# Optimization experiments

Measured on AMD Instinct MI355X. Metric: run time of the kernel, lower is better.

## Reference

```python
import jax, jax.numpy as jnp
import numpy as np

S, B, D, H = 512, 2048, 64, 128  # seqLength, batchSize, inputDim, hiddenDim


def setup_inputs() -> dict:
    key = jax.random.key(0)
    ks = jax.random.split(key, 6)
    return {
        "x": jax.random.normal(ks[0], (S, B, D), dtype=jnp.float32),
        "h0": jax.random.normal(ks[1], (B, H), dtype=jnp.float32) * 0.1,
        # nn.Linear(64,128) params
        "W_ih": jax.random.normal(ks[2], (H, D), dtype=jnp.float32) / np.sqrt(D).astype(np.float32),
        "b_ih": jax.random.normal(ks[3], (H,), dtype=jnp.float32) * 0.01,
        # nn.Linear(128,128) params
        "W_hh": jax.random.normal(ks[4], (H, H), dtype=jnp.float32) / np.sqrt(H).astype(np.float32),
        "b_hh": jax.random.normal(ks[5], (H,), dtype=jnp.float32) * 0.01,
    }


def reference(x, h0, W_ih, b_ih, W_hh, b_hh):
    """Elman-style cell from the source, scanned over the sequence:
       wih_x = Linear_ih(x_t) * h
       whh   = Linear_hh(wih_x) * h
       h'    = tanh(wih_x + whh)
    Returns final hidden state [B, H]."""

    def cell(h, x_t):
        wih_x = (x_t @ W_ih.T + b_ih) * h          # [B, H]
        whh = (wih_x @ W_hh.T + b_hh) * h           # [B, H]
        h_new = jnp.tanh(wih_x + whh)
        return h_new, None

    h_final, _ = jax.lax.scan(cell, h0, x)  # x: [S, B, D]
    return h_final
```

## Files before the change

kernel.cpp:

```cpp
#include <hip/hip_runtime.h>
#include <cmath>

#define SEQ 512
#define BATCH 2048
#define DIM 64
#define HID 128
#define SB (BATCH * DIM)


#define R4(M) M(0) M(1) M(2) M(3)
#define R8(M) R4(M) M(4) M(5) M(6) M(7)

#define PIN4(F_) asm volatile("" : "+v"(F_.x), "+v"(F_.y), "+v"(F_.z), "+v"(F_.w));
#define PIN1(F_) asm volatile("" : "+v"(F_));

__device__ __forceinline__ float fast_tanh(float z) {
    const float e = __expf(2.0f * z);
    return 1.0f - 2.0f * __builtin_amdgcn_rcpf(e + 1.0f);
}

__global__ __launch_bounds__(512)
__attribute__((amdgpu_waves_per_eu(4, 8)))
void rnn_kernel(const float* __restrict__ x,
                const float* __restrict__ h0,
                const float* __restrict__ W_ih,
                const float* __restrict__ b_ih,
                const float* __restrict__ W_hh,
                const float* __restrict__ b_hh,
                float* __restrict__ out) {
    __shared__ __align__(16) float xs[2][4][64];
    __shared__ __align__(16) float part1[4][HID];
    __shared__ __align__(16) float part2[4][HID];
    __shared__ __align__(16) float act[HID];

    const int tid = threadIdx.x;
    const int b = blockIdx.x;
    const int j = tid & 127;
    const int kq = tid >> 7;
    const int lane = tid & 63;

    const float4* wip = (const float4*)(W_ih + j * DIM + kq * 16);
#define DECL_WI(i) float4 wi##i = wip[i]; PIN4(wi##i)
    R4(DECL_WI)
    const float4* whp = (const float4*)(W_hh + j * HID + kq * 32);
#define DECL_WH(i) float4 wh##i = whp[i]; PIN4(wh##i)
    R8(DECL_WH)

    float bi = b_ih[j];  PIN1(bi)
    float bh = b_hh[j];  PIN1(bh)
    float h = h0[b * HID + j];

    const float* xgl = x + (size_t)b * DIM + (size_t)(lane >> 4) * SB
                         + (size_t)((lane & 15) * 4);
    float* xlds = &xs[0][lane >> 4][(lane & 15) * 4];

    *(float4*)(xlds)       = *(const float4*)(xgl);
    *(float4*)(xlds + 256) = *(const float4*)(xgl + 4 * (size_t)SB);
    float4 xr = *(const float4*)(xgl + 8 * (size_t)SB);
    const float* xnext = xgl + 12 * (size_t)SB;

    float wihx;
    {
        float pP = 0.f, pQ = 0.f;
        const float4* xv = (const float4*)&xs[0][0][kq * 16];
#define G1P(c) { const float4 v_ = xv[c]; \
        pP += wi##c.x * v_.x; pP += wi##c.y * v_.y; \
        pQ += wi##c.z * v_.z; pQ += wi##c.w * v_.w; }
        R4(G1P)
        part1[kq][j] = pP + pQ;
    }
    asm volatile("s_waitcnt lgkmcnt(0)\n\ts_barrier" ::: "memory");
    {
        const float* p1 = &part1[0][j];
        wihx = (((p1[0] + p1[128]) + (p1[256] + p1[384])) + bi) * h;
        if (kq == 0) act[j] = wihx;
    }
    asm volatile("s_waitcnt lgkmcnt(0)\n\ts_barrier" ::: "memory");

#pragma unroll 1
    for (int t = 0; t < SEQ; ++t) {
        if ((t & 3) == 3) {
            if (t + 5 < SEQ) {
                *(float4*)(xlds + ((t >> 2) & 1) * 256) = xr;
                if (t + 9 < SEQ) {
                    xr = *(const float4*)xnext;
                    xnext += 4 * (size_t)SB;
                }
            }
        }

        float qP = 0.f, qQ = 0.f;
        const float4* av = (const float4*)&act[kq * 32];
#define G2P(c) { const float4 v_ = av[c]; \
        qP += wh##c.x * v_.x; qP += wh##c.y * v_.y; \
        qQ += wh##c.z * v_.z; qQ += wh##c.w * v_.w; }
        R8(G2P)

        const int tn = t + 1;
        if (tn < SEQ) {
            float pP = 0.f, pQ = 0.f;
            const float4* xv = (const float4*)&xs[(tn >> 2) & 1][tn & 3][kq * 16];
#define G1N(c) { const float4 v_ = xv[c]; \
            pP += wi##c.x * v_.x; pP += wi##c.y * v_.y; \
            pQ += wi##c.z * v_.z; pQ += wi##c.w * v_.w; }
            R4(G1N)
            part1[kq][j] = pP + pQ;
        }
        part2[kq][j] = qP + qQ;
        asm volatile("s_waitcnt lgkmcnt(0)\n\ts_barrier" ::: "memory");

        {
            const float* p2 = &part2[0][j];
            const float whh = (((p2[0] + p2[128]) + (p2[256] + p2[384])) + bh) * h;
            h = fast_tanh(wihx + whh);
            if (tn < SEQ) {
                const float* p1 = &part1[0][j];
                wihx = (((p1[0] + p1[128]) + (p1[256] + p1[384])) + bi) * h;
                if (kq == 0) act[j] = wihx;
            }
        }
        asm volatile("s_waitcnt lgkmcnt(0)\n\ts_barrier" ::: "memory");
    }

    if (kq == 0) out[b * HID + j] = h;
}

extern "C" void kernel_launch(void* const* d_in, const int* in_sizes, int n_in,
                              void* d_out, int out_size, void* d_ws, size_t ws_size,
                              hipStream_t stream) {
    const float* x    = (const float*)d_in[0];
    const float* h0   = (const float*)d_in[1];
    const float* W_ih = (const float*)d_in[2];
    const float* b_ih = (const float*)d_in[3];
    const float* W_hh = (const float*)d_in[4];
    const float* b_hh = (const float*)d_in[5];
    float* out = (float*)d_out;

    dim3 grid(BATCH);
    dim3 block(512);
    rnn_kernel<<<grid, block, 0, stream>>>(x, h0, W_ih, b_ih, W_hh, b_hh, out);
}
```

Measured before the change: 1.870 ms.

## Process two batch rows per block to reuse register-resident weights

Each block now handles two batch rows instead of one. The register-held W_ih/W_hh slices are applied to both rows' inputs and activations, which halves the grid and the per-row barrier and weight-load overhead. The x staging buffer is reorganised to hold two rows across two timesteps, and the waves-per-EU cap is lowered to allow more registers. The cost is more register pressure and LDS traffic per step, and fewer blocks in flight to hide the serial recurrence latency.

Result: slower. 4.973 ms (+166.0%).

```diff
diff --git a/kernel.cpp b/kernel.cpp
--- a/kernel.cpp
+++ b/kernel.cpp
@@ -20,7 +20,7 @@
 }
 
 __global__ __launch_bounds__(512)
-__attribute__((amdgpu_waves_per_eu(4, 8)))
+__attribute__((amdgpu_waves_per_eu(4, 6)))
 void rnn_kernel(const float* __restrict__ x,
                 const float* __restrict__ h0,
                 const float* __restrict__ W_ih,
@@ -28,16 +28,16 @@
                 const float* __restrict__ W_hh,
                 const float* __restrict__ b_hh,
                 float* __restrict__ out) {
-    __shared__ __align__(16) float xs[2][4][64];
-    __shared__ __align__(16) float part1[4][HID];
-    __shared__ __align__(16) float part2[4][HID];
-    __shared__ __align__(16) float act[HID];
+    __shared__ __align__(16) float xs[2][256];
+    __shared__ __align__(16) float part1[2][4][HID];
+    __shared__ __align__(16) float part2[2][4][HID];
+    __shared__ __align__(16) float act[2][HID];
 
     const int tid = threadIdx.x;
-    const int b = blockIdx.x;
     const int j = tid & 127;
     const int kq = tid >> 7;
     const int lane = tid & 63;
+    const int b0 = blockIdx.x * 2;
 
     const float4* wip = (const float4*)(W_ih + j * DIM + kq * 16);
 #define DECL_WI(i) float4 wi##i = wip[i]; PIN4(wi##i)
@@ -48,81 +48,91 @@
 
     float bi = b_ih[j];  PIN1(bi)
     float bh = b_hh[j];  PIN1(bh)
-    float h = h0[b * HID + j];
+    float h = (kq < 2) ? h0[(b0 + kq) * HID + j] : 0.0f;
 
-    const float* xgl = x + (size_t)b * DIM + (size_t)(lane >> 4) * SB
+    const float* xgl = x + (size_t)b0 * DIM + (size_t)(lane >> 5) * SB
+                         + (size_t)(((lane >> 4) & 1) * DIM)
                          + (size_t)((lane & 15) * 4);
-    float* xlds = &xs[0][lane >> 4][(lane & 15) * 4];
+    float* xldsW = &xs[0][lane * 4];
 
-    *(float4*)(xlds)       = *(const float4*)(xgl);
-    *(float4*)(xlds + 256) = *(const float4*)(xgl + 4 * (size_t)SB);
-    float4 xr = *(const float4*)(xgl + 8 * (size_t)SB);
-    const float* xnext = xgl + 12 * (size_t)SB;
+    *(float4*)(xldsW)       = *(const float4*)(xgl);
+    *(float4*)(xldsW + 256) = *(const float4*)(xgl + 2 * (size_t)SB);
+    float4 xr = *(const float4*)(xgl + 4 * (size_t)SB);
+    const float* xnext = xgl + 6 * (size_t)SB;
 
-    float wihx;
+    float wihx = 0.0f;
     {
-        float pP = 0.f, pQ = 0.f;
-        const float4* xv = (const float4*)&xs[0][0][kq * 16];
-#define G1P(c) { const float4 v_ = xv[c]; \
-        pP += wi##c.x * v_.x; pP += wi##c.y * v_.y; \
-        pQ += wi##c.z * v_.z; pQ += wi##c.w * v_.w; }
-        R4(G1P)
-        part1[kq][j] = pP + pQ;
+        float pP0 = 0.f, pQ0 = 0.f, pP1 = 0.f, pQ1 = 0.f;
+        const float* xb = &xs[0][kq * 16];
+        const float4* xv0 = (const float4*)(xb);
+        const float4* xv1 = (const float4*)(xb + 64);
+#define G1N(c) { const float4 u_ = xv0[c]; const float4 v_ = xv1[c]; \
+        pP0 += wi##c.x * u_.x; pP0 += wi##c.y * u_.y; \
+        pQ0 += wi##c.z * u_.z; pQ0 += wi##c.w * u_.w; \
+        pP1 += wi##c.x * v_.x; pP1 += wi##c.y * v_.y; \
+        pQ1 += wi##c.z * v_.z; pQ1 += wi##c.w * v_.w; }
+        R4(G1N)
+        part1[0][kq][j] = pP0 + pQ0;
+        part1[1][kq][j] = pP1 + pQ1;
     }
     asm volatile("s_waitcnt lgkmcnt(0)\n\ts_barrier" ::: "memory");
-    {
-        const float* p1 = &part1[0][j];
+    if (kq < 2) {
+        const float* p1 = &part1[kq][0][j];
         wihx = (((p1[0] + p1[128]) + (p1[256] + p1[384])) + bi) * h;
-        if (kq == 0) act[j] = wihx;
+        act[kq][j] = wihx;
     }
     asm volatile("s_waitcnt lgkmcnt(0)\n\ts_barrier" ::: "memory");
 
-#pragma unroll 1
+#pragma unroll 2
     for (int t = 0; t < SEQ; ++t) {
-        if ((t & 3) == 3) {
-            if (t + 5 < SEQ) {
-                *(float4*)(xlds + ((t >> 2) & 1) * 256) = xr;
-                if (t + 9 < SEQ) {
+        if ((t & 1) == 1) {
+            if (t + 3 < SEQ) {
+                *(float4*)(xldsW + ((t >> 1) & 1) * 256) = xr;
+                if (t + 5 < SEQ) {
                     xr = *(const float4*)xnext;
-                    xnext += 4 * (size_t)SB;
+                    xnext += 2 * (size_t)SB;
                 }
             }
         }
 
-        float qP = 0.f, qQ = 0.f;
-        const float4* av = (const float4*)&act[kq * 32];
-#define G2P(c) { const float4 v_ = av[c]; \
-        qP += wh##c.x * v_.x; qP += wh##c.y * v_.y; \
-        qQ += wh##c.z * v_.z; qQ += wh##c.w * v_.w; }
+        float qP0 = 0.f, qQ0 = 0.f, qP1 = 0.f, qQ1 = 0.f;
+        const float4* av0 = (const float4*)&act[0][kq * 32];
+        const float4* av1 = (const float4*)&act[1][kq * 32];
+#define G2P(c) { const float4 u_ = av0[c]; const float4 v_ = av1[c]; \
+        qP0 += wh##c.x * u_.x; qP0 += wh##c.y * u_.y; \
+        qQ0 += wh##c.z * u_.z; qQ0 += wh##c.w * u_.w; \
+        qP1 += wh##c.x * v_.x; qP1 += wh##c.y * v_.y; \
+        qQ1 += wh##c.z * v_.z; qQ1 += wh##c.w * v_.w; }
         R8(G2P)
 
         const int tn = t + 1;
         if (tn < SEQ) {
-            float pP = 0.f, pQ = 0.f;
-            const float4* xv = (const float4*)&xs[(tn >> 2) & 1][tn & 3][kq * 16];
-#define G1N(c) { const float4 v_ = xv[c]; \
-            pP += wi##c.x * v_.x; pP += wi##c.y * v_.y; \
-            pQ += wi##c.z * v_.z; pQ += wi##c.w * v_.w; }
+            float pP0 = 0.f, pQ0 = 0.f, pP1 = 0.f, pQ1 = 0.f;
+            const float* xb = &xs[(tn >> 1) & 1][(tn & 1) * 128 + kq * 16];
+            const float4* xv0 = (const float4*)(xb);
+            const float4* xv1 = (const float4*)(xb + 64);
             R4(G1N)
-            part1[kq][j] = pP + pQ;
+            part1[0][kq][j] = pP0 + pQ0;
+            part1[1][kq][j] = pP1 + pQ1;
         }
-        part2[kq][j] = qP + qQ;
+        part2[0][kq][j] = qP0 + qQ0;
+        part2[1][kq][j] = qP1 + qQ1;
         asm volatile("s_waitcnt lgkmcnt(0)\n\ts_barrier" ::: "memory");
 
-        {
-            const float* p2 = &part2[0][j];
+        if (kq < 2) {
+            const float* p2 = &part2[kq][0][j];
             const float whh = (((p2[0] + p2[128]) + (p2[256] + p2[384])) + bh) * h;
             h = fast_tanh(wihx + whh);
             if (tn < SEQ) {
-                const float* p1 = &part1[0][j];
+                const float* p1 = &part1[kq][0][j];
                 wihx = (((p1[0] + p1[128]) + (p1[256] + p1[384])) + bi) * h;
-                if (kq == 0) act[j] = wihx;
+                act[kq][j] = wihx;
             }
         }
         asm volatile("s_waitcnt lgkmcnt(0)\n\ts_barrier" ::: "memory");
     }
 
-    if (kq == 0) out[b * HID + j] = h;
+    if (kq < 2) out[(b0 + kq) * HID + j] = h;
 }
 
 extern "C" void kernel_launch(void* const* d_in, const int* in_sizes, int n_in,
@@ -136,7 +146,7 @@
     const float* b_hh = (const float*)d_in[5];
     float* out = (float*)d_out;
 
-    dim3 grid(BATCH);
+    dim3 grid(BATCH / 2);
     dim3 block(512);
     rnn_kernel<<<grid, block, 0, stream>>>(x, h0, W_ih, b_ih, W_hh, b_hh, out);
 }
```
